# Performance work log

Hardware: AMD Instinct MI355X
Metric: run time of the kernel (lower is better)

The kernel has to match this reference:

```python
import jax, jax.numpy as jnp
import numpy as np

N_HEADS = 16
NEG_BIAS = -1000000000.0


def setup_inputs() -> dict:
    key = jax.random.key(0)
    k1, k2, k3, k4 = jax.random.split(key, 4)
    B, S, D = 2, 2048, 1024
    queries = jax.random.normal(k1, (B, S, D), dtype=jnp.float32)
    keys = jax.random.normal(k2, (B, S, D), dtype=jnp.float32)
    values = jax.random.normal(k3, (B, S, D), dtype=jnp.float32)
    mask = jax.random.randint(k4, (B, S, S), 0, 2, dtype=jnp.int32)
    return {"queries": queries, "keys": keys, "values": values, "mask": mask}


def _split_heads(x):
    B, S, D = x.shape
    return x.reshape(B, S, N_HEADS, D // N_HEADS).transpose(0, 2, 1, 3)  # [B,H,S,d]


def reference(queries, keys, values, mask):
    q = _split_heads(queries)   # [B,H,Sq,d]
    k = _split_heads(keys)      # [B,H,Sk,d]
    v = _split_heads(values)    # [B,H,Sk,d]
    d_head = q.shape[-1]
    # scaled dot product similarity
    sim = jnp.einsum('bhqd,bhkd->bhqk', q, k) / jnp.sqrt(jnp.float32(d_head))
    # additive mask (softmax attention function -> non-hadamard)
    bias = NEG_BIAS * (1.0 - mask.astype(sim.dtype))[:, None]  # [B,1,Sq,Sk]
    sim = sim + bias
    # softmax with max-subtraction (numerically stable, as in original)
    weights = jax.nn.softmax(sim, axis=-1)
    out = jnp.einsum('bhqk,bhkd->bhqd', weights, v)  # [B,H,Sq,d]
    B, H, Sq, d = out.shape
    return out.transpose(0, 2, 1, 3).reshape(B, Sq, H * d)
```

## Files before the change

kernel.cpp:

```cpp
#include <hip/hip_runtime.h>

#define S_LEN 2048
#define D_MODEL 1024
#define DH 64
#define BQ 128
#define BK 128
#define ZSCALE 0.18033688f

using short8 = __attribute__((ext_vector_type(8))) short;
using s4v    = __attribute__((ext_vector_type(4))) short;
using f32x4  = __attribute__((ext_vector_type(4))) float;
using u32x4  = __attribute__((ext_vector_type(4))) unsigned int;

#define BMM(a, b, c) __builtin_amdgcn_mfma_f32_16x16x32_bf16((a), (b), (c), 0, 0, 0)

__device__ __forceinline__ unsigned short f2bf(float x) {
    union { float f; unsigned int u; } c; c.f = x;
    unsigned int u = c.u;
    u += 0x7fffu + ((u >> 16) & 1u);
    return (unsigned short)(u >> 16);
}

__global__ __launch_bounds__(256) void cvt_fused(const float* __restrict__ V,
                                                 const int* __restrict__ M,
                                                 const float* __restrict__ K,
                                                 unsigned short* __restrict__ VT,
                                                 unsigned long long* __restrict__ Mb,
                                                 unsigned short* __restrict__ KB) {
    const int blk = blockIdx.x;
    const int tid = threadIdx.x;
    if (blk < 1024) {
        __shared__ float tsF[64][65];
        const int b  = blk >> 9;
        const int h  = (blk >> 5) & 15;
        const int s0 = (blk & 31) * 64;
        #pragma unroll
        for (int it = 0; it < 2; ++it) {
            int seg = tid + it * 256;
            int s = seg >> 3, d8 = (seg & 7) << 3;
            const float* p = V + (size_t)(b * S_LEN + s0 + s) * D_MODEL + h * DH + d8;
            f32x4 a = *(const f32x4*)p;
            f32x4 c = *(const f32x4*)(p + 4);
            #pragma unroll
            for (int j = 0; j < 4; ++j) { tsF[s][d8 + j] = a[j]; tsF[s][d8 + 4 + j] = c[j]; }
        }
        __syncthreads();
        #pragma unroll
        for (int it = 0; it < 2; ++it) {
            int seg = tid + it * 256;
            int d = seg >> 3, s8 = (seg & 7) << 3;
            short8 w;
            #pragma unroll
            for (int j = 0; j < 8; ++j) w[j] = (short)f2bf(tsF[s8 + j][d]);
            *(short8*)(VT + ((size_t)((b * 16 + h) * 64 + d)) * S_LEN + s0 + s8) = w;
        }
    } else if (blk < 2048) {
        const int pb   = blk - 1024;
        const int wave = tid >> 6, lane = tid & 63;
        const int row  = pb * 4 + wave;
        const int* mp  = M + (size_t)row * S_LEN;
        #pragma unroll 4
        for (int it = 0; it < 32; ++it) {
            int m = mp[it * 64 + lane];
            unsigned long long bal = __ballot(m != 0);
            if (lane == 0) Mb[(size_t)row * 32 + it] = bal;
        }
    } else {
        size_t base = (size_t)(blk - 2048) * 4096;
        #pragma unroll
        for (int it = 0; it < 4; ++it) {
            size_t i = base + ((size_t)(it * 256 + tid)) * 4;
            f32x4 a = *(const f32x4*)(K + i);
            s4v w;
            #pragma unroll
            for (int j = 0; j < 4; ++j) w[j] = (short)f2bf(a[j]);
            *(s4v*)(KB + i) = w;
        }
    }
}

__global__ __launch_bounds__(256) void mha_fwd_v15(
    const float* __restrict__ Q,
    const float* __restrict__ K,
    const unsigned short* __restrict__ KB,
    const unsigned short* __restrict__ VT,
    const unsigned long long* __restrict__ Mb,
    float* __restrict__ O,
    int kbf)
{
    __shared__ alignas(16) unsigned short Ks[BK][64];
    __shared__ alignas(16) unsigned short Vt[DH][128];

    const int blk0 = blockIdx.x;
    const int blk  = ((blk0 & 7) << 6) | (blk0 >> 3);

    const int b   = blk >> 8;
    const int h   = (blk >> 4) & 15;
    const int qbase = (blk & 15) * BQ;
    const int bh  = b * 16 + h;

    const int tid  = threadIdx.x;
    const int wave = tid >> 6;
    const int lane = tid & 63;
    const int n16  = lane & 15;
    const int quad = lane >> 4;
    const int bq   = quad << 3;
    const int n7   = n16 & 7;

    const int srow = tid >> 3;
    const int prow = (((srow >> 2) & 1) << 4) | (((srow >> 3) & 3) << 2) | (srow & 3);
    const int vrow = tid >> 4;

    const int kwcol = (((tid & 7) ^ (prow & 7)) << 3);
    const int vwcol = (((tid & 15) ^ vrow) << 3);
    const int krc0  = ((quad ^ n7) << 3);
    const int krc1  = krc0 ^ 32;
    int vrc[4];
    #pragma unroll
    for (int kc = 0; kc < 4; ++kc) vrc[kc] = (((kc * 4 + quad) ^ n16) << 3);

    short8 qf[2][2];
    #pragma unroll
    for (int qg = 0; qg < 2; ++qg) {
        const size_t qoff = (size_t)(b * S_LEN + qbase + wave * 32 + qg * 16 + n16) * D_MODEL
                          + h * DH + quad * 8;
        f32x4 a0 = *(const f32x4*)(Q + qoff);
        f32x4 a1 = *(const f32x4*)(Q + qoff + 4);
        f32x4 a2 = *(const f32x4*)(Q + qoff + 32);
        f32x4 a3 = *(const f32x4*)(Q + qoff + 36);
        short8 q0, q1;
        #pragma unroll
        for (int j = 0; j < 4; ++j) {
            q0[j] = (short)f2bf(a0[j] * ZSCALE); q0[4 + j] = (short)f2bf(a1[j] * ZSCALE);
            q1[j] = (short)f2bf(a2[j] * ZSCALE); q1[4 + j] = (short)f2bf(a3[j] * ZSCALE);
        }
        qf[qg][0] = q0; qf[qg][1] = q1;
    }

    const short8 ones = {0x3F80,0x3F80,0x3F80,0x3F80,0x3F80,0x3F80,0x3F80,0x3F80};

    f32x4 o[2][4], o4[2];
    #pragma unroll
    for (int qg = 0; qg < 2; ++qg) {
        #pragma unroll
        for (int dg = 0; dg < 4; ++dg) o[qg][dg] = f32x4{0.f,0.f,0.f,0.f};
        o4[qg] = f32x4{0.f,0.f,0.f,0.f};
    }

    const unsigned long long* mrow[2];
    #pragma unroll
    for (int qg = 0; qg < 2; ++qg)
        mrow[qg] = Mb + (size_t)(b * S_LEN + qbase + wave * 32 + qg * 16 + n16) * 32;

    const size_t kbase = (size_t)(b * S_LEN) * D_MODEL + h * DH;
    const size_t vbase = (size_t)(bh * 64) * S_LEN;

    short8 ka[4], va[4];
    unsigned long long mw[2][2];
    if (kbf) {
        #pragma unroll
        for (int i = 0; i < 4; ++i)
            ka[i] = *(const short8*)(KB + kbase + (size_t)(i * 32 + srow) * D_MODEL + ((tid & 7) << 3));
    } else {
        #pragma unroll
        for (int i = 0; i < 4; ++i) {
            const float* kp = K + kbase + (size_t)(i * 32 + srow) * D_MODEL + ((tid & 7) << 3);
            f32x4 p0 = *(const f32x4*)kp, p1 = *(const f32x4*)(kp + 4);
            short8 w;
            #pragma unroll
            for (int j = 0; j < 4; ++j) { w[j] = (short)f2bf(p0[j]); w[4 + j] = (short)f2bf(p1[j]); }
            ka[i] = w;
        }
    }
    #pragma unroll
    for (int i = 0; i < 4; ++i)
        va[i] = *(const short8*)(VT + vbase + (size_t)(vrow + 16 * i) * S_LEN + ((tid & 15) << 3));
    #pragma unroll
    for (int qg = 0; qg < 2; ++qg) { mw[qg][0] = mrow[qg][0]; mw[qg][1] = mrow[qg][1]; }

    for (int kb = 0; kb < S_LEN; kb += BK) {
        __builtin_amdgcn_s_barrier();
        __builtin_amdgcn_sched_barrier(0);

        #pragma unroll
        for (int i = 0; i < 4; ++i) {
            *(short8*)&Ks[prow + 32 * i][kwcol] = ka[i];
            *(short8*)&Vt[vrow + 16 * i][vwcol] = va[i];
        }

        const int kn = kb + BK;
        const bool more = kn < S_LEN;
        short8 nka[4], nva[4];
        unsigned long long nmw[2][2];
        if (more) {
            if (kbf) {
                #pragma unroll
                for (int i = 0; i < 4; ++i)
                    nka[i] = *(const short8*)(KB + kbase + (size_t)(kn + i * 32 + srow) * D_MODEL + ((tid & 7) << 3));
            } else {
                #pragma unroll
                for (int i = 0; i < 4; ++i) {
                    const float* kp = K + kbase + (size_t)(kn + i * 32 + srow) * D_MODEL + ((tid & 7) << 3);
                    f32x4 p0 = *(const f32x4*)kp, p1 = *(const f32x4*)(kp + 4);
                    short8 w;
                    #pragma unroll
                    for (int j = 0; j < 4; ++j) { w[j] = (short)f2bf(p0[j]); w[4 + j] = (short)f2bf(p1[j]); }
                    nka[i] = w;
                }
            }
            #pragma unroll
            for (int i = 0; i < 4; ++i)
                nva[i] = *(const short8*)(VT + vbase + (size_t)(vrow + 16 * i) * S_LEN + kn + ((tid & 15) << 3));
            const int wi = kn >> 6;
            #pragma unroll
            for (int qg = 0; qg < 2; ++qg) { nmw[qg][0] = mrow[qg][wi]; nmw[qg][1] = mrow[qg][wi + 1]; }
        }

        unsigned int am[2][4];
        #pragma unroll
        for (int qg = 0; qg < 2; ++qg) {
            am[qg][0] = ((unsigned int)mw[qg][0]) >> bq;
            am[qg][1] = ((unsigned int)(mw[qg][0] >> 32)) >> bq;
            am[qg][2] = ((unsigned int)mw[qg][1]) >> bq;
            am[qg][3] = ((unsigned int)(mw[qg][1] >> 32)) >> bq;
        }

        asm volatile("s_waitcnt lgkmcnt(0)" ::: "memory");
        __builtin_amdgcn_s_barrier();
        __builtin_amdgcn_sched_barrier(0);

        u32x4 Af[2][4];
        auto QKCT = [&](int ct) {
            short8 kf0 = *(const short8*)&Ks[ct * 16 + n16][krc0];
            short8 kf1 = *(const short8*)&Ks[ct * 16 + n16][krc1];
            f32x4 sA = {0.f,0.f,0.f,0.f}, sB = sA;
            sA = BMM(kf0, qf[0][0], sA); sA = BMM(kf1, qf[0][1], sA);
            sB = BMM(kf0, qf[1][0], sB); sB = BMM(kf1, qf[1][1], sB);
            unsigned int puA[4], puB[4];
            #pragma unroll
            for (int r = 0; r < 4; ++r) {
                puA[r] = __float_as_uint(__builtin_amdgcn_exp2f(sA[r]));
                puB[r] = __float_as_uint(__builtin_amdgcn_exp2f(sB[r]));
            }
            const int sel = ct >> 1, sb = (ct & 1) * 4, kc = ct >> 1, ub = (ct & 1) * 2;
            unsigned int nibA = (am[0][sel] >> sb) & 0xFu;
            unsigned int nibB = (am[1][sel] >> sb) & 0xFu;
            unsigned int m8A = ((nibA * 0x00204081u) & 0x01010101u) * 0xFFu;
            unsigned int m8B = ((nibB * 0x00204081u) & 0x01010101u) * 0xFFu;
            Af[0][kc][ub + 0] = __builtin_amdgcn_perm(puA[1], puA[0], 0x07060302u)
                              & __builtin_amdgcn_perm(0u, m8A, 0x01010000u);
            Af[0][kc][ub + 1] = __builtin_amdgcn_perm(puA[3], puA[2], 0x07060302u)
                              & __builtin_amdgcn_perm(0u, m8A, 0x03030202u);
            Af[1][kc][ub + 0] = __builtin_amdgcn_perm(puB[1], puB[0], 0x07060302u)
                              & __builtin_amdgcn_perm(0u, m8B, 0x01010000u);
            Af[1][kc][ub + 1] = __builtin_amdgcn_perm(puB[3], puB[2], 0x07060302u)
                              & __builtin_amdgcn_perm(0u, m8B, 0x03030202u);
        };
        auto PVKC = [&](int kc) {
            short8 v0 = *(const short8*)&Vt[      n16][vrc[kc]];
            short8 v1 = *(const short8*)&Vt[16 + n16][vrc[kc]];
            short8 v2 = *(const short8*)&Vt[32 + n16][vrc[kc]];
            short8 v3 = *(const short8*)&Vt[48 + n16][vrc[kc]];
            union { u32x4 u; short8 s; } c0, c1;
            c0.u = Af[0][kc]; c1.u = Af[1][kc];
            o[0][0] = BMM(c0.s, v0, o[0][0]); o[0][1] = BMM(c0.s, v1, o[0][1]);
            o[0][2] = BMM(c0.s, v2, o[0][2]); o[0][3] = BMM(c0.s, v3, o[0][3]);
            o4[0]   = BMM(c0.s, ones, o4[0]);
            o[1][0] = BMM(c1.s, v0, o[1][0]); o[1][1] = BMM(c1.s, v1, o[1][1]);
            o[1][2] = BMM(c1.s, v2, o[1][2]); o[1][3] = BMM(c1.s, v3, o[1][3]);
            o4[1]   = BMM(c1.s, ones, o4[1]);
        };

        __builtin_amdgcn_s_setprio(1);
        QKCT(0); QKCT(1);
        PVKC(0);
        QKCT(2); QKCT(3);
        PVKC(1);
        QKCT(4); QKCT(5);
        PVKC(2);
        QKCT(6); QKCT(7);
        PVKC(3);
        __builtin_amdgcn_s_setprio(0);

        if (more) {
            #pragma unroll
            for (int i = 0; i < 4; ++i) { ka[i] = nka[i]; va[i] = nva[i]; }
            #pragma unroll
            for (int qg = 0; qg < 2; ++qg) { mw[qg][0] = nmw[qg][0]; mw[qg][1] = nmw[qg][1]; }
        }
    }

    #pragma unroll
    for (int qg = 0; qg < 2; ++qg) {
        #pragma unroll
        for (int r = 0; r < 4; ++r) {
            float rl = 1.f / o4[qg][r];
            size_t row = (size_t)(b * S_LEN + qbase + wave * 32 + qg * 16 + quad * 4 + r);
            float* op = O + row * D_MODEL + h * DH + n16;
            op[0]  = o[qg][0][r] * rl;
            op[16] = o[qg][1][r] * rl;
            op[32] = o[qg][2][r] * rl;
            op[48] = o[qg][3][r] * rl;
        }
    }
}

extern "C" void kernel_launch(void* const* d_in, const int* in_sizes, int n_in,
                              void* d_out, int out_size, void* d_ws, size_t ws_size,
                              hipStream_t stream) {
    const float* Q = (const float*)d_in[0];
    const float* K = (const float*)d_in[1];
    const float* V = (const float*)d_in[2];
    const int*   M = (const int*)d_in[3];
    float*       O = (float*)d_out;

    const size_t NEL = (size_t)2 * S_LEN * D_MODEL;
    const size_t VT_BYTES = NEL * sizeof(unsigned short);
    const size_t KB_BYTES = NEL * sizeof(unsigned short);
    const size_t MB_BYTES = (size_t)2 * S_LEN * 32 * 8;

    if (ws_size >= VT_BYTES + KB_BYTES + MB_BYTES) {
        unsigned short* VT = (unsigned short*)d_ws;
        unsigned short* KB = (unsigned short*)((char*)d_ws + VT_BYTES);
        unsigned long long* Mb = (unsigned long long*)((char*)d_ws + VT_BYTES + KB_BYTES);
        hipLaunchKernelGGL(cvt_fused, dim3(3072), dim3(256), 0, stream, V, M, K, VT, Mb, KB);
        hipLaunchKernelGGL(mha_fwd_v15, dim3(512), dim3(256), 0, stream,
                           Q, K, KB, VT, Mb, O, 1);
    } else {
        unsigned short* VT = (unsigned short*)d_ws;
        unsigned long long* Mb = (unsigned long long*)((char*)d_ws + VT_BYTES);
        hipLaunchKernelGGL(cvt_fused, dim3(2048), dim3(256), 0, stream, V, M, K, VT, Mb, (unsigned short*)0);
        hipLaunchKernelGGL(mha_fwd_v15, dim3(512), dim3(256), 0, stream,
                           Q, K, (const unsigned short*)0, VT, Mb, O, 0);
    }
}
```

Baseline: 171.0 us.

## Double-buffer K/V shared tiles and interleave staging with MFMA compute

Splits the K and V shared-memory tiles into two ping-pong buffers and unrolls the key loop by two with register sets A/B. While one buffer is consumed by the QK/PV MFMAs, the previously loaded tile is written into the other buffer between compute chunks. This removes one of the two block barriers per key block and the serial staging phase before compute. In exchange it doubles LDS use and adds register pressure from the two prefetch register sets.

```diff
diff --git a/kernel.cpp b/kernel.cpp
--- a/kernel.cpp
+++ b/kernel.cpp
@@ -13,6 +13,9 @@
 using u32x4  = __attribute__((ext_vector_type(4))) unsigned int;
 
 #define BMM(a, b, c) __builtin_amdgcn_mfma_f32_16x16x32_bf16((a), (b), (c), 0, 0, 0)
+#define LGKM_BAR() do { asm volatile("s_waitcnt lgkmcnt(0)" ::: "memory"); \
+                        __builtin_amdgcn_s_barrier(); \
+                        __builtin_amdgcn_sched_barrier(0); } while (0)
 
 __device__ __forceinline__ unsigned short f2bf(float x) {
     union { float f; unsigned int u; } c; c.f = x;
@@ -79,7 +82,7 @@
     }
 }
 
-__global__ __launch_bounds__(256) void mha_fwd_v15(
+__global__ __launch_bounds__(256) void mha_fwd_v16(
     const float* __restrict__ Q,
     const float* __restrict__ K,
     const unsigned short* __restrict__ KB,
@@ -88,8 +91,8 @@
     float* __restrict__ O,
     int kbf)
 {
-    __shared__ alignas(16) unsigned short Ks[BK][64];
-    __shared__ alignas(16) unsigned short Vt[DH][128];
+    __shared__ alignas(16) unsigned short Ks[2][BK][64];
+    __shared__ alignas(16) unsigned short Vt[2][DH][128];
 
     const int blk0 = blockIdx.x;
     const int blk  = ((blk0 & 7) << 6) | (blk0 >> 3);
@@ -155,68 +158,33 @@
     const size_t kbase = (size_t)(b * S_LEN) * D_MODEL + h * DH;
     const size_t vbase = (size_t)(bh * 64) * S_LEN;
 
-    short8 ka[4], va[4];
-    unsigned long long mw[2][2];
-    if (kbf) {
+    short8 kaA[4], vaA[4], kaB[4], vaB[4];
+    unsigned long long mwA[2][2], mwB[2][2];
+
+    auto LD = [&](int kb2, short8 (&ka)[4], short8 (&va)[4], unsigned long long (&mw)[2][2]) {
+        if (kbf) {
+            #pragma unroll
+            for (int i = 0; i < 4; ++i)
+                ka[i] = *(const short8*)(KB + kbase + (size_t)(kb2 + i * 32 + srow) * D_MODEL + ((tid & 7) << 3));
+        } else {
+            #pragma unroll
+            for (int i = 0; i < 4; ++i) {
+                const float* kp = K + kbase + (size_t)(kb2 + i * 32 + srow) * D_MODEL + ((tid & 7) << 3);
+                f32x4 p0 = *(const f32x4*)kp, p1 = *(const f32x4*)(kp + 4);
+                short8 w;
+                #pragma unroll
+                for (int j = 0; j < 4; ++j) { w[j] = (short)f2bf(p0[j]); w[4 + j] = (short)f2bf(p1[j]); }
+                ka[i] = w;
+            }
+        }
         #pragma unroll
         for (int i = 0; i < 4; ++i)
-            ka[i] = *(const short8*)(KB + kbase + (size_t)(i * 32 + srow) * D_MODEL + ((tid & 7) << 3));
-    } else {
-        #pragma unroll
-        for (int i = 0; i < 4; ++i) {
-            const float* kp = K + kbase + (size_t)(i * 32 + srow) * D_MODEL + ((tid & 7) << 3);
-            f32x4 p0 = *(const f32x4*)kp, p1 = *(const f32x4*)(kp + 4);
-            short8 w;
-            #pragma unroll
-            for (int j = 0; j < 4; ++j) { w[j] = (short)f2bf(p0[j]); w[4 + j] = (short)f2bf(p1[j]); }
-            ka[i] = w;
-        }
-    }
-    #pragma unroll
-    for (int i = 0; i < 4; ++i)
-        va[i] = *(const short8*)(VT + vbase + (size_t)(vrow + 16 * i) * S_LEN + ((tid & 15) << 3));
-    #pragma unroll
-    for (int qg = 0; qg < 2; ++qg) { mw[qg][0] = mrow[qg][0]; mw[qg][1] = mrow[qg][1]; }
-
-    for (int kb = 0; kb < S_LEN; kb += BK) {
-        __builtin_amdgcn_s_barrier();
-        __builtin_amdgcn_sched_barrier(0);
-
-        #pragma unroll
-        for (int i = 0; i < 4; ++i) {
-            *(short8*)&Ks[prow + 32 * i][kwcol] = ka[i];
-            *(short8*)&Vt[vrow + 16 * i][vwcol] = va[i];
-        }
-
-        const int kn = kb + BK;
-        const bool more = kn < S_LEN;
-        short8 nka[4], nva[4];
-        unsigned long long nmw[2][2];
-        if (more) {
-            if (kbf) {
-                #pragma unroll
-                for (int i = 0; i < 4; ++i)
-                    nka[i] = *(const short8*)(KB + kbase + (size_t)(kn + i * 32 + srow) * D_MODEL + ((tid & 7) << 3));
-            } else {
-                #pragma unroll
-                for (int i = 0; i < 4; ++i) {
-                    const float* kp = K + kbase + (size_t)(kn + i * 32 + srow) * D_MODEL + ((tid & 7) << 3);
-                    f32x4 p0 = *(const f32x4*)kp, p1 = *(const f32x4*)(kp + 4);
-                    short8 w;
-                    #pragma unroll
-                    for (int j = 0; j < 4; ++j) { w[j] = (short)f2bf(p0[j]); w[4 + j] = (short)f2bf(p1[j]); }
-                    nka[i] = w;
-                }
-            }
-            #pragma unroll
-            for (int i = 0; i < 4; ++i)
-                nva[i] = *(const short8*)(VT + vbase + (size_t)(vrow + 16 * i) * S_LEN + kn + ((tid & 15) << 3));
-            const int wi = kn >> 6;
-            #pragma unroll
-            for (int qg = 0; qg < 2; ++qg) { nmw[qg][0] = mrow[qg][wi]; nmw[qg][1] = mrow[qg][wi + 1]; }
-        }
-
-        unsigned int am[2][4];
+            va[i] = *(const short8*)(VT + vbase + (size_t)(vrow + 16 * i) * S_LEN + kb2 + ((tid & 15) << 3));
+        const int wi = kb2 >> 6;
+        #pragma unroll
+        for (int qg = 0; qg < 2; ++qg) { mw[qg][0] = mrow[qg][wi]; mw[qg][1] = mrow[qg][wi + 1]; }
+    };
+    auto MKAM = [&](unsigned long long (&mw)[2][2], unsigned int (&am)[2][4]) {
         #pragma unroll
         for (int qg = 0; qg < 2; ++qg) {
             am[qg][0] = ((unsigned int)mw[qg][0]) >> bq;
@@ -224,71 +192,85 @@
             am[qg][2] = ((unsigned int)mw[qg][1]) >> bq;
             am[qg][3] = ((unsigned int)(mw[qg][1] >> 32)) >> bq;
         }
-
-        asm volatile("s_waitcnt lgkmcnt(0)" ::: "memory");
-        __builtin_amdgcn_s_barrier();
-        __builtin_amdgcn_sched_barrier(0);
-
+    };
+    auto QKCT = [&](int pb, int ct, unsigned int (&am)[2][4], u32x4 (&Af)[2][4]) {
+        short8 kf0 = *(const short8*)&Ks[pb][ct * 16 + n16][krc0];
+        short8 kf1 = *(const short8*)&Ks[pb][ct * 16 + n16][krc1];
+        f32x4 sA = {0.f,0.f,0.f,0.f}, sB = sA;
+        sA = BMM(kf0, qf[0][0], sA); sA = BMM(kf1, qf[0][1], sA);
+        sB = BMM(kf0, qf[1][0], sB); sB = BMM(kf1, qf[1][1], sB);
+        unsigned int puA[4], puB[4];
+        #pragma unroll
+        for (int r = 0; r < 4; ++r) {
+            puA[r] = __float_as_uint(__builtin_amdgcn_exp2f(sA[r]));
+            puB[r] = __float_as_uint(__builtin_amdgcn_exp2f(sB[r]));
+        }
+        const int sel = ct >> 1, sb = (ct & 1) * 4, kc = ct >> 1, ub = (ct & 1) * 2;
+        unsigned int nibA = (am[0][sel] >> sb) & 0xFu;
+        unsigned int nibB = (am[1][sel] >> sb) & 0xFu;
+        unsigned int m8A = ((nibA * 0x00204081u) & 0x01010101u) * 0xFFu;
+        unsigned int m8B = ((nibB * 0x00204081u) & 0x01010101u) * 0xFFu;
+        Af[0][kc][ub + 0] = __builtin_amdgcn_perm(puA[1], puA[0], 0x07060302u)
+                          & __builtin_amdgcn_perm(0u, m8A, 0x01010000u);
+        Af[0][kc][ub + 1] = __builtin_amdgcn_perm(puA[3], puA[2], 0x07060302u)
+                          & __builtin_amdgcn_perm(0u, m8A, 0x03030202u);
+        Af[1][kc][ub + 0] = __builtin_amdgcn_perm(puB[1], puB[0], 0x07060302u)
+                          & __builtin_amdgcn_perm(0u, m8B, 0x01010000u);
+        Af[1][kc][ub + 1] = __builtin_amdgcn_perm(puB[3], puB[2], 0x07060302u)
+                          & __builtin_amdgcn_perm(0u, m8B, 0x03030202u);
+    };
+    auto PVKC = [&](int pb, int kc, u32x4 (&Af)[2][4]) {
+        short8 v0 = *(const short8*)&Vt[pb][      n16][vrc[kc]];
+        short8 v1 = *(const short8*)&Vt[pb][16 + n16][vrc[kc]];
+        short8 v2 = *(const short8*)&Vt[pb][32 + n16][vrc[kc]];
+        short8 v3 = *(const short8*)&Vt[pb][48 + n16][vrc[kc]];
+        union { u32x4 u; short8 s; } c0, c1;
+        c0.u = Af[0][kc]; c1.u = Af[1][kc];
+        o[0][0] = BMM(c0.s, v0, o[0][0]); o[0][1] = BMM(c0.s, v1, o[0][1]);
+        o[0][2] = BMM(c0.s, v2, o[0][2]); o[0][3] = BMM(c0.s, v3, o[0][3]);
+        o4[0]   = BMM(c0.s, ones, o4[0]);
+        o[1][0] = BMM(c1.s, v0, o[1][0]); o[1][1] = BMM(c1.s, v1, o[1][1]);
+        o[1][2] = BMM(c1.s, v2, o[1][2]); o[1][3] = BMM(c1.s, v3, o[1][3]);
+        o4[1]   = BMM(c1.s, ones, o4[1]);
+    };
+    auto STG = [&](int pb, short8 (&ka)[4], short8 (&va)[4], int i) {
+        *(short8*)&Ks[pb][prow + 32 * i][kwcol] = ka[i];
+        *(short8*)&Vt[pb][vrow + 16 * i][vwcol] = va[i];
+    };
+    auto BODY = [&](int pb, unsigned long long (&mwC)[2][2],
+                    int ldkb, short8 (&lka)[4], short8 (&lva)[4],
+                    unsigned long long (&lmw)[2][2], bool doLoad,
+                    short8 (&ska)[4], short8 (&sva)[4], bool doStage) {
+        unsigned int am[2][4]; MKAM(mwC, am);
+        if (doLoad) LD(ldkb, lka, lva, lmw);
         u32x4 Af[2][4];
-        auto QKCT = [&](int ct) {
-            short8 kf0 = *(const short8*)&Ks[ct * 16 + n16][krc0];
-            short8 kf1 = *(const short8*)&Ks[ct * 16 + n16][krc1];
-            f32x4 sA = {0.f,0.f,0.f,0.f}, sB = sA;
-            sA = BMM(kf0, qf[0][0], sA); sA = BMM(kf1, qf[0][1], sA);
-            sB = BMM(kf0, qf[1][0], sB); sB = BMM(kf1, qf[1][1], sB);
-            unsigned int puA[4], puB[4];
-            #pragma unroll
-            for (int r = 0; r < 4; ++r) {
-                puA[r] = __float_as_uint(__builtin_amdgcn_exp2f(sA[r]));
-                puB[r] = __float_as_uint(__builtin_amdgcn_exp2f(sB[r]));
-            }
-            const int sel = ct >> 1, sb = (ct & 1) * 4, kc = ct >> 1, ub = (ct & 1) * 2;
-            unsigned int nibA = (am[0][sel] >> sb) & 0xFu;
-            unsigned int nibB = (am[1][sel] >> sb) & 0xFu;
-            unsigned int m8A = ((nibA * 0x00204081u) & 0x01010101u) * 0xFFu;
-            unsigned int m8B = ((nibB * 0x00204081u) & 0x01010101u) * 0xFFu;
-            Af[0][kc][ub + 0] = __builtin_amdgcn_perm(puA[1], puA[0], 0x07060302u)
-                              & __builtin_amdgcn_perm(0u, m8A, 0x01010000u);
-            Af[0][kc][ub + 1] = __builtin_amdgcn_perm(puA[3], puA[2], 0x07060302u)
-                              & __builtin_amdgcn_perm(0u, m8A, 0x03030202u);
-            Af[1][kc][ub + 0] = __builtin_amdgcn_perm(puB[1], puB[0], 0x07060302u)
-                              & __builtin_amdgcn_perm(0u, m8B, 0x01010000u);
-            Af[1][kc][ub + 1] = __builtin_amdgcn_perm(puB[3], puB[2], 0x07060302u)
-                              & __builtin_amdgcn_perm(0u, m8B, 0x03030202u);
-        };
-        auto PVKC = [&](int kc) {
-            short8 v0 = *(const short8*)&Vt[      n16][vrc[kc]];
-            short8 v1 = *(const short8*)&Vt[16 + n16][vrc[kc]];
-            short8 v2 = *(const short8*)&Vt[32 + n16][vrc[kc]];
-            short8 v3 = *(const short8*)&Vt[48 + n16][vrc[kc]];
-            union { u32x4 u; short8 s; } c0, c1;
-            c0.u = Af[0][kc]; c1.u = Af[1][kc];
-            o[0][0] = BMM(c0.s, v0, o[0][0]); o[0][1] = BMM(c0.s, v1, o[0][1]);
-            o[0][2] = BMM(c0.s, v2, o[0][2]); o[0][3] = BMM(c0.s, v3, o[0][3]);
-            o4[0]   = BMM(c0.s, ones, o4[0]);
-            o[1][0] = BMM(c1.s, v0, o[1][0]); o[1][1] = BMM(c1.s, v1, o[1][1]);
-            o[1][2] = BMM(c1.s, v2, o[1][2]); o[1][3] = BMM(c1.s, v3, o[1][3]);
-            o4[1]   = BMM(c1.s, ones, o4[1]);
-        };
-
         __builtin_amdgcn_s_setprio(1);
-        QKCT(0); QKCT(1);
-        PVKC(0);
-        QKCT(2); QKCT(3);
-        PVKC(1);
-        QKCT(4); QKCT(5);
-        PVKC(2);
-        QKCT(6); QKCT(7);
-        PVKC(3);
+        QKCT(pb, 0, am, Af); QKCT(pb, 1, am, Af); PVKC(pb, 0, Af);
+        if (doStage) STG(pb ^ 1, ska, sva, 0);
+        QKCT(pb, 2, am, Af); QKCT(pb, 3, am, Af); PVKC(pb, 1, Af);
+        if (doStage) STG(pb ^ 1, ska, sva, 1);
+        QKCT(pb, 4, am, Af); QKCT(pb, 5, am, Af); PVKC(pb, 2, Af);
+        if (doStage) STG(pb ^ 1, ska, sva, 2);
+        QKCT(pb, 6, am, Af); QKCT(pb, 7, am, Af); PVKC(pb, 3, Af);
+        if (doStage) STG(pb ^ 1, ska, sva, 3);
         __builtin_amdgcn_s_setprio(0);
-
-        if (more) {
-            #pragma unroll
-            for (int i = 0; i < 4; ++i) { ka[i] = nka[i]; va[i] = nva[i]; }
-            #pragma unroll
-            for (int qg = 0; qg < 2; ++qg) { mw[qg][0] = nmw[qg][0]; mw[qg][1] = nmw[qg][1]; }
-        }
-    }
+    };
+
+    LD(0, kaA, vaA, mwA);
+    #pragma unroll
+    for (int i = 0; i < 4; ++i) STG(0, kaA, vaA, i);
+    LD(BK, kaB, vaB, mwB);
+    LGKM_BAR();
+
+    for (int it = 0; it < 7; ++it) {
+        BODY(0, mwA, (2 * it + 2) * BK, kaA, vaA, mwA, true, kaB, vaB, true);
+        LGKM_BAR();
+        BODY(1, mwB, (2 * it + 3) * BK, kaB, vaB, mwB, true, kaA, vaA, true);
+        LGKM_BAR();
+    }
+    BODY(0, mwA, 0, kaA, vaA, mwA, false, kaB, vaB, true);
+    LGKM_BAR();
+    BODY(1, mwB, 0, kaB, vaB, mwB, false, kaA, vaA, false);
 
     #pragma unroll
     for (int qg = 0; qg < 2; ++qg) {
@@ -324,13 +306,13 @@
         unsigned short* KB = (unsigned short*)((char*)d_ws + VT_BYTES);
         unsigned long long* Mb = (unsigned long long*)((char*)d_ws + VT_BYTES + KB_BYTES);
         hipLaunchKernelGGL(cvt_fused, dim3(3072), dim3(256), 0, stream, V, M, K, VT, Mb, KB);
-        hipLaunchKernelGGL(mha_fwd_v15, dim3(512), dim3(256), 0, stream,
+        hipLaunchKernelGGL(mha_fwd_v16, dim3(512), dim3(256), 0, stream,
                            Q, K, KB, VT, Mb, O, 1);
     } else {
         unsigned short* VT = (unsigned short*)d_ws;
         unsigned long long* Mb = (unsigned long long*)((char*)d_ws + VT_BYTES);
         hipLaunchKernelGGL(cvt_fused, dim3(2048), dim3(256), 0, stream, V, M, K, VT, Mb, (unsigned short*)0);
-        hipLaunchKernelGGL(mha_fwd_v15, dim3(512), dim3(256), 0, stream,
+        hipLaunchKernelGGL(mha_fwd_v16, dim3(512), dim3(256), 0, stream,
                            Q, K, (const unsigned short*)0, VT, Mb, O, 0);
     }
 }
```

Result: no change. 171.5 us (+0.3%).

## Split key range across two blocks per query tile and add combine kernel

Applied to the files above, without the earlier changes.

The attention kernel can now split each (batch, head, query-tile) job into two halves of the key sequence, launching 1024 blocks instead of 512. Each half writes unnormalized partial outputs and row sums to workspace, and a new combine kernel adds them and normalizes into the output. The aim is more parallelism and better CU fill on the GPU. The cost is an extra kernel launch and roughly 33 MB of partial-result traffic written and read back. The split path runs only when the workspace is large enough.

```diff
diff --git a/kernel.cpp b/kernel.cpp
--- a/kernel.cpp
+++ b/kernel.cpp
@@ -79,25 +79,33 @@
     }
 }
 
-__global__ __launch_bounds__(256) void mha_fwd_v15(
+__global__ __launch_bounds__(256) void mha_fwd_v18(
     const float* __restrict__ Q,
     const float* __restrict__ K,
     const unsigned short* __restrict__ KB,
     const unsigned short* __restrict__ VT,
     const unsigned long long* __restrict__ Mb,
     float* __restrict__ O,
-    int kbf)
+    float* __restrict__ PO,
+    float* __restrict__ PL,
+    int kbf, int split_mode)
 {
     __shared__ alignas(16) unsigned short Ks[BK][64];
     __shared__ alignas(16) unsigned short Vt[DH][128];
 
     const int blk0 = blockIdx.x;
-    const int blk  = ((blk0 & 7) << 6) | (blk0 >> 3);
-
-    const int b   = blk >> 8;
-    const int h   = (blk >> 4) & 15;
-    const int qbase = (blk & 15) * BQ;
+    int blk, b, h, qt, split;
+    if (split_mode) {
+        blk = ((blk0 & 7) << 7) | (blk0 >> 3);
+        b = blk >> 9; h = (blk >> 5) & 15; qt = (blk >> 1) & 15; split = blk & 1;
+    } else {
+        blk = ((blk0 & 7) << 6) | (blk0 >> 3);
+        b = blk >> 8; h = (blk >> 4) & 15; qt = blk & 15; split = 0;
+    }
+    const int qbase = qt * BQ;
     const int bh  = b * 16 + h;
+    const int kb0 = split * (S_LEN / 2);
+    const int kbend = split_mode ? kb0 + S_LEN / 2 : S_LEN;
 
     const int tid  = threadIdx.x;
     const int wave = tid >> 6;
@@ -160,11 +168,11 @@
     if (kbf) {
         #pragma unroll
         for (int i = 0; i < 4; ++i)
-            ka[i] = *(const short8*)(KB + kbase + (size_t)(i * 32 + srow) * D_MODEL + ((tid & 7) << 3));
+            ka[i] = *(const short8*)(KB + kbase + (size_t)(kb0 + i * 32 + srow) * D_MODEL + ((tid & 7) << 3));
     } else {
         #pragma unroll
         for (int i = 0; i < 4; ++i) {
-            const float* kp = K + kbase + (size_t)(i * 32 + srow) * D_MODEL + ((tid & 7) << 3);
+            const float* kp = K + kbase + (size_t)(kb0 + i * 32 + srow) * D_MODEL + ((tid & 7) << 3);
             f32x4 p0 = *(const f32x4*)kp, p1 = *(const f32x4*)(kp + 4);
             short8 w;
             #pragma unroll
@@ -174,11 +182,14 @@
     }
     #pragma unroll
     for (int i = 0; i < 4; ++i)
-        va[i] = *(const short8*)(VT + vbase + (size_t)(vrow + 16 * i) * S_LEN + ((tid & 15) << 3));
-    #pragma unroll
-    for (int qg = 0; qg < 2; ++qg) { mw[qg][0] = mrow[qg][0]; mw[qg][1] = mrow[qg][1]; }
-
-    for (int kb = 0; kb < S_LEN; kb += BK) {
+        va[i] = *(const short8*)(VT + vbase + (size_t)(vrow + 16 * i) * S_LEN + kb0 + ((tid & 15) << 3));
+    {
+        const int wi = kb0 >> 6;
+        #pragma unroll
+        for (int qg = 0; qg < 2; ++qg) { mw[qg][0] = mrow[qg][wi]; mw[qg][1] = mrow[qg][wi + 1]; }
+    }
+
+    for (int kb = kb0; kb < kbend; kb += BK) {
         __builtin_amdgcn_s_barrier();
         __builtin_amdgcn_sched_barrier(0);
 
@@ -189,7 +200,7 @@
         }
 
         const int kn = kb + BK;
-        const bool more = kn < S_LEN;
+        const bool more = kn < kbend;
         short8 nka[4], nva[4];
         unsigned long long nmw[2][2];
         if (more) {
@@ -290,18 +301,62 @@
         }
     }
 
-    #pragma unroll
-    for (int qg = 0; qg < 2; ++qg) {
-        #pragma unroll
-        for (int r = 0; r < 4; ++r) {
-            float rl = 1.f / o4[qg][r];
-            size_t row = (size_t)(b * S_LEN + qbase + wave * 32 + qg * 16 + quad * 4 + r);
-            float* op = O + row * D_MODEL + h * DH + n16;
-            op[0]  = o[qg][0][r] * rl;
-            op[16] = o[qg][1][r] * rl;
-            op[32] = o[qg][2][r] * rl;
-            op[48] = o[qg][3][r] * rl;
-        }
+    if (PO) {
+        const int pblk = (bh * 16 + qt) * 2 + split;
+        float* pp = PO + (size_t)pblk * (BQ * DH);
+        float* pl = PL + (size_t)pblk * BQ;
+        #pragma unroll
+        for (int qg = 0; qg < 2; ++qg) {
+            #pragma unroll
+            for (int r = 0; r < 4; ++r) {
+                const int rowin = wave * 32 + qg * 16 + quad * 4 + r;
+                float* op = pp + rowin * DH + n16;
+                op[0]  = o[qg][0][r];
+                op[16] = o[qg][1][r];
+                op[32] = o[qg][2][r];
+                op[48] = o[qg][3][r];
+                if (n16 == 0) pl[rowin] = o4[qg][r];
+            }
+        }
+    } else {
+        #pragma unroll
+        for (int qg = 0; qg < 2; ++qg) {
+            #pragma unroll
+            for (int r = 0; r < 4; ++r) {
+                float rl = 1.f / o4[qg][r];
+                size_t row = (size_t)(b * S_LEN + qbase + wave * 32 + qg * 16 + quad * 4 + r);
+                float* op = O + row * D_MODEL + h * DH + n16;
+                op[0]  = o[qg][0][r] * rl;
+                op[16] = o[qg][1][r] * rl;
+                op[32] = o[qg][2][r] * rl;
+                op[48] = o[qg][3][r] * rl;
+            }
+        }
+    }
+}
+
+__global__ __launch_bounds__(256) void combine_split(
+    const float* __restrict__ PO, const float* __restrict__ PL,
+    float* __restrict__ O)
+{
+    const int tq = blockIdx.x;
+    const int b = tq >> 8, h = (tq >> 4) & 15, qt = tq & 15;
+    const float* p0 = PO + (size_t)tq * 2 * (BQ * DH);
+    const float* p1 = p0 + BQ * DH;
+    const float* l0 = PL + (size_t)tq * 2 * BQ;
+    const float* l1 = l0 + BQ;
+    const int t = threadIdx.x;
+    #pragma unroll
+    for (int k = 0; k < 8; ++k) {
+        const int e   = (t + k * 256) * 4;
+        const int row = e >> 6, col = e & 63;
+        f32x4 a = *(const f32x4*)(p0 + e);
+        f32x4 c = *(const f32x4*)(p1 + e);
+        const float rl = 1.f / (l0[row] + l1[row]);
+        f32x4 r;
+        #pragma unroll
+        for (int j = 0; j < 4; ++j) r[j] = (a[j] + c[j]) * rl;
+        *(f32x4*)(O + (size_t)(b * S_LEN + qt * BQ + row) * D_MODEL + h * DH + col) = r;
     }
 }
 
@@ -318,19 +373,31 @@
     const size_t VT_BYTES = NEL * sizeof(unsigned short);
     const size_t KB_BYTES = NEL * sizeof(unsigned short);
     const size_t MB_BYTES = (size_t)2 * S_LEN * 32 * 8;
-
-    if (ws_size >= VT_BYTES + KB_BYTES + MB_BYTES) {
+    const size_t PO_BYTES = (size_t)512 * 2 * BQ * DH * 4;
+    const size_t PL_BYTES = (size_t)512 * 2 * BQ * 4;
+
+    if (ws_size >= VT_BYTES + KB_BYTES + MB_BYTES + PO_BYTES + PL_BYTES) {
+        unsigned short* VT = (unsigned short*)d_ws;
+        unsigned short* KB = (unsigned short*)((char*)d_ws + VT_BYTES);
+        unsigned long long* Mb = (unsigned long long*)((char*)d_ws + VT_BYTES + KB_BYTES);
+        float* PO = (float*)((char*)d_ws + VT_BYTES + KB_BYTES + MB_BYTES);
+        float* PL = (float*)((char*)d_ws + VT_BYTES + KB_BYTES + MB_BYTES + PO_BYTES);
+        hipLaunchKernelGGL(cvt_fused, dim3(3072), dim3(256), 0, stream, V, M, K, VT, Mb, KB);
+        hipLaunchKernelGGL(mha_fwd_v18, dim3(1024), dim3(256), 0, stream,
+                           Q, K, KB, VT, Mb, O, PO, PL, 1, 1);
+        hipLaunchKernelGGL(combine_split, dim3(512), dim3(256), 0, stream, PO, PL, O);
+    } else if (ws_size >= VT_BYTES + KB_BYTES + MB_BYTES) {
         unsigned short* VT = (unsigned short*)d_ws;
         unsigned short* KB = (unsigned short*)((char*)d_ws + VT_BYTES);
         unsigned long long* Mb = (unsigned long long*)((char*)d_ws + VT_BYTES + KB_BYTES);
         hipLaunchKernelGGL(cvt_fused, dim3(3072), dim3(256), 0, stream, V, M, K, VT, Mb, KB);
-        hipLaunchKernelGGL(mha_fwd_v15, dim3(512), dim3(256), 0, stream,
-                           Q, K, KB, VT, Mb, O, 1);
+        hipLaunchKernelGGL(mha_fwd_v18, dim3(512), dim3(256), 0, stream,
+                           Q, K, KB, VT, Mb, O, (float*)0, (float*)0, 1, 0);
     } else {
         unsigned short* VT = (unsigned short*)d_ws;
         unsigned long long* Mb = (unsigned long long*)((char*)d_ws + VT_BYTES);
         hipLaunchKernelGGL(cvt_fused, dim3(2048), dim3(256), 0, stream, V, M, K, VT, Mb, (unsigned short*)0);
-        hipLaunchKernelGGL(mha_fwd_v15, dim3(512), dim3(256), 0, stream,
-                           Q, K, (const unsigned short*)0, VT, Mb, O, 0);
+        hipLaunchKernelGGL(mha_fwd_v18, dim3(512), dim3(256), 0, stream,
+                           Q, K, (const unsigned short*)0, VT, Mb, O, (float*)0, (float*)0, 0, 0);
     }
 }
```

New measurement: 181.4 us. +6.1%, slower.
